# Kernel optimization log

Hardware: AMD Instinct MI355X
Metric: run time of the kernel (lower is better)

Reference implementation:

```python
import jax, jax.numpy as jnp
import numpy as np

D_MODEL = 1024
NUM_HEADS = 16
D_K = D_MODEL // NUM_HEADS
THETA = 10000.0
MAX_SEQ_LEN = 2048
BATCH = 2
SEQ = 2048


def setup_inputs() -> dict:
    key = jax.random.key(0)
    ks = jax.random.split(key, 5)
    std = np.sqrt(2.0 / (D_MODEL + D_MODEL)).astype(np.float32)
    x = jax.random.normal(ks[0], (BATCH, SEQ, D_MODEL), dtype=jnp.float32)
    Wq = jax.random.normal(ks[1], (D_MODEL, D_MODEL), dtype=jnp.float32) * std
    Wk = jax.random.normal(ks[2], (D_MODEL, D_MODEL), dtype=jnp.float32) * std
    Wv = jax.random.normal(ks[3], (D_MODEL, D_MODEL), dtype=jnp.float32) * std
    Wo = jax.random.normal(ks[4], (D_MODEL, D_MODEL), dtype=jnp.float32) * std
    token_positions = jnp.arange(SEQ, dtype=jnp.int32)
    return {"x": x, "token_positions": token_positions,
            "Wq": Wq, "Wk": Wk, "Wv": Wv, "Wo": Wo}


def _rope_tables(positions):
    # freqs: [d_k/2]; angles: [seq, d_k/2]
    freqs = 1.0 / (THETA ** (jnp.arange(0, D_K, 2, dtype=jnp.float32) / D_K))
    angles = positions.astype(jnp.float32)[:, None] * freqs[None, :]
    return jnp.cos(angles), jnp.sin(angles)


def _apply_rope(t, cos, sin):
    # t: [b, h, s, d_k]; cos/sin: [s, d_k/2]; interleaved pair rotation
    x1 = t[..., 0::2]
    x2 = t[..., 1::2]
    r1 = x1 * cos - x2 * sin
    r2 = x1 * sin + x2 * cos
    return jnp.stack([r1, r2], axis=-1).reshape(t.shape)


def reference(x, token_positions, Wq, Wk, Wv, Wo):
    b, s, _ = x.shape
    # projections: y = x W^T
    q = jnp.einsum('bsi,oi->bso', x, Wq)
    k = jnp.einsum('bsi,oi->bso', x, Wk)
    v = jnp.einsum('bsi,oi->bso', x, Wv)
    # split heads: [b, h, s, d]
    q = q.reshape(b, s, NUM_HEADS, D_K).transpose(0, 2, 1, 3)
    k = k.reshape(b, s, NUM_HEADS, D_K).transpose(0, 2, 1, 3)
    v = v.reshape(b, s, NUM_HEADS, D_K).transpose(0, 2, 1, 3)
    cos, sin = _rope_tables(token_positions)
    q = _apply_rope(q, cos, sin)
    k = _apply_rope(k, cos, sin)
    scale = jnp.asarray(D_K, jnp.float32) ** 0.5
    scores = jnp.einsum('bhqd,bhkd->bhqk', q, k) / scale
    causal = jnp.tril(jnp.ones((s, s), dtype=bool))
    scores = jnp.where(causal, scores, -jnp.inf)
    attn = jax.nn.softmax(scores.astype(jnp.float32), axis=-1).astype(scores.dtype)
    out = jnp.einsum('bhqk,bhkd->bhqd', attn, v)
    out = out.transpose(0, 2, 1, 3).reshape(b, s, D_MODEL)
    return jnp.einsum('bsi,oi->bso', out, Wo)
```

## Files before the change

kernel.cpp:

```cpp
#include <hip/hip_runtime.h>
#include <stdint.h>

#define D_MODEL 1024
#define NH      16
#define DKH     64
#define SEQLEN  2048
#define BATCH   2
#define KDIM    1024

typedef __attribute__((ext_vector_type(8))) short          short8;
typedef __attribute__((ext_vector_type(4))) short          bf16x4;
typedef __attribute__((ext_vector_type(8))) unsigned short ushort8;
typedef __attribute__((ext_vector_type(4))) unsigned short usht4;
typedef __attribute__((ext_vector_type(4))) float          f32x4;

#define QSCALE 0.18033688011112042f

__device__ __forceinline__ unsigned short f2bf(float f) {
    union { float f; unsigned u; } v; v.f = f;
    unsigned u = v.u;
    unsigned r = (u + 0x7FFFu + ((u >> 16) & 1u)) >> 16;
    return (unsigned short)r;
}
__device__ __forceinline__ unsigned fbits(float f) {
    union { float f; unsigned u; } v; v.f = f; return v.u;
}

__device__ __forceinline__ void gload_lds16(const unsigned short* g, unsigned short* l) {
    __builtin_amdgcn_global_load_lds(
        (__attribute__((address_space(1))) void*)(g),
        (__attribute__((address_space(3))) void*)(l), 16, 0, 0);
}

__global__ void cvt_all(const float* __restrict__ X,  const float* __restrict__ Wq,
                        const float* __restrict__ Wk, const float* __restrict__ Wv,
                        const float* __restrict__ Wo, const int* __restrict__ pos,
                        unsigned short* __restrict__ Xb,  unsigned short* __restrict__ Wqb,
                        unsigned short* __restrict__ Wkb, unsigned short* __restrict__ Wvb,
                        unsigned short* __restrict__ Wob, float2* __restrict__ tbl) {
    const int z = blockIdx.y;
    if (z == 5) {
        int i = blockIdx.x * 256 + threadIdx.x;
        if (i < 65536) {
            int s = i >> 5, j = i & 31;
            float freq = expf(-((float)(2 * j) * (1.0f / 64.0f)) * 9.210340371976184f);
            float ang = (float)pos[s] * freq;
            float sn, cn;
            sincosf(ang, &sn, &cn);
            tbl[i] = make_float2(cn, sn);
        }
        return;
    }
    const float* src; unsigned short* dst; int n;
    if (z == 0)      { src = X;  dst = Xb;  n = 4194304; }
    else if (z == 1) { src = Wq; dst = Wqb; n = 1048576; }
    else if (z == 2) { src = Wk; dst = Wkb; n = 1048576; }
    else if (z == 3) { src = Wv; dst = Wvb; n = 1048576; }
    else             { src = Wo; dst = Wob; n = 1048576; }
    int i = (blockIdx.x * 256 + threadIdx.x) * 8;
    if (i >= n) return;
    float4 a = *(const float4*)(src + i);
    float4 b = *(const float4*)(src + i + 4);
    ushort8 o;
    o[0] = f2bf(a.x); o[1] = f2bf(a.y); o[2] = f2bf(a.z); o[3] = f2bf(a.w);
    o[4] = f2bf(b.x); o[5] = f2bf(b.y); o[6] = f2bf(b.z); o[7] = f2bf(b.w);
    *(ushort8*)(dst + i) = o;
}

__device__ __forceinline__ void gemm_core_128(
    const unsigned short* __restrict__ A, const unsigned short* __restrict__ W,
    unsigned short* a_lds, unsigned short* b_lds,
    int m0, int n0, f32x4 acc[4][4])
{
    const int tid  = threadIdx.x;
    const int lane = tid & 63;
    const int w    = tid >> 6;
    const int quad = lane >> 4;
    const int l16  = lane & 15;
    const int wm   = w & 1, wn = w >> 1;

    const int row_in = lane >> 3;
    const int cg     = ((lane & 7) ^ row_in) * 8;

    #pragma unroll
    for (int mi = 0; mi < 4; mi++)
        #pragma unroll
        for (int ni = 0; ni < 4; ni++) {
            f32x4 z = {0.f, 0.f, 0.f, 0.f};
            acc[mi][ni] = z;
        }

    const int x7 = l16 & 7;

    for (int kk = 0; kk < KDIM; kk += 64) {
        __syncthreads();
        #pragma unroll
        for (int j = 0; j < 4; ++j) {
            int c = w * 4 + j;
            gload_lds16(A + (size_t)(m0 + c * 8 + row_in) * KDIM + kk + cg, &a_lds[c * 512]);
            gload_lds16(W + (size_t)(n0 + c * 8 + row_in) * KDIM + kk + cg, &b_lds[c * 512]);
        }
        __syncthreads();

        short8 af[2][4], bf[2][4];
        #pragma unroll
        for (int kk2 = 0; kk2 < 2; kk2++)
            #pragma unroll
            for (int i = 0; i < 4; i++) {
                int g = (kk2 * 4 + quad) ^ x7;
                af[kk2][i] = *(const short8*)&a_lds[(wm * 64 + i * 16 + l16) * 64 + g * 8];
                bf[kk2][i] = *(const short8*)&b_lds[(wn * 64 + i * 16 + l16) * 64 + g * 8];
            }
        #pragma unroll
        for (int kk2 = 0; kk2 < 2; kk2++)
            #pragma unroll
            for (int mi = 0; mi < 4; mi++)
                #pragma unroll
                for (int ni = 0; ni < 4; ni++)
                    acc[mi][ni] = __builtin_amdgcn_mfma_f32_16x16x32_bf16(af[kk2][mi], bf[kk2][ni], acc[mi][ni], 0, 0, 0);
    }
}

__global__ __launch_bounds__(256, 2)
void gemm_qkv(const unsigned short* __restrict__ X,
              const unsigned short* __restrict__ Wq,
              const unsigned short* __restrict__ Wk,
              const unsigned short* __restrict__ Wv,
              const float2* __restrict__ tbl,
              unsigned short* __restrict__ q_ws,
              unsigned short* __restrict__ k_ws,
              unsigned short* __restrict__ v_ws)
{
    __shared__ __align__(16) unsigned short a_lds[128 * 64];
    __shared__ __align__(16) unsigned short b_lds[128 * 64];
    __shared__ __align__(16) unsigned short t_lds[32 * 136];

    const int z = blockIdx.z;
    const unsigned short* W = (z == 0) ? Wq : ((z == 1) ? Wk : Wv);
    const int m0 = blockIdx.x * 128, n0 = blockIdx.y * 128;

    f32x4 acc[4][4];
    gemm_core_128(X, W, a_lds, b_lds, m0, n0, acc);

    const int tid  = threadIdx.x;
    const int lane = tid & 63;
    const int w    = tid >> 6;
    const int quad = lane >> 4;
    const int l16  = lane & 15;
    const int wm   = w & 1, wn = w >> 1;

    if (z == 2) {
        const int bx = m0 >> 11;
        const int c_local_w = wn * 16 + l16;
        const int rd_c = tid >> 3;
        const int rd_s = (tid & 7) * 16;
        #pragma unroll
        for (int ni = 0; ni < 4; ni++) {
            __syncthreads();
            #pragma unroll
            for (int mi = 0; mi < 4; mi++) {
                usht4 v4;
                #pragma unroll
                for (int r = 0; r < 4; r++) v4[r] = f2bf(acc[mi][ni][r]);
                *(usht4*)&t_lds[c_local_w * 136 + wm * 64 + mi * 16 + quad * 4] = v4;
            }
            __syncthreads();
            int col = n0 + (rd_c >> 4) * 64 + ni * 16 + (rd_c & 15);
            int h = col >> 6, d = col & 63;
            size_t base = (size_t)(bx * NH + h) * DKH * SEQLEN + (size_t)d * SEQLEN
                        + (m0 & 2047) + rd_s;
            ushort8 x0 = *(ushort8*)&t_lds[rd_c * 136 + rd_s];
            ushort8 x1 = *(ushort8*)&t_lds[rd_c * 136 + rd_s + 8];
            *(ushort8*)&v_ws[base]     = x0;
            *(ushort8*)&v_ws[base + 8] = x1;
        }
    } else {
        unsigned short* dst = (z == 0) ? q_ws : k_ws;
        const float sc = (z == 0) ? QSCALE : 1.0f;
        #pragma unroll
        for (int mi = 0; mi < 4; mi++)
            #pragma unroll
            for (int ni = 0; ni < 4; ni++)
                #pragma unroll
                for (int r = 0; r < 4; r++) {
                    int row = m0 + wm * 64 + mi * 16 + quad * 4 + r;
                    int col = n0 + wn * 64 + ni * 16 + l16;
                    int b = row >> 11, s = row & 2047;
                    int h = col >> 6,  d = col & 63;
                    float val = acc[mi][ni][r];
                    float other = __shfl_xor(val, 1);
                    float2 cs = tbl[s * 32 + (d >> 1)];
                    float rv = (d & 1) ? (other * cs.y + val * cs.x)
                                       : (val * cs.x - other * cs.y);
                    dst[(size_t)(b * NH + h) * SEQLEN * DKH + (size_t)s * DKH + d] =
                        f2bf(rv * sc);
                }
    }
}

__global__ __launch_bounds__(256, 2)
void attn_kernel(const unsigned short* __restrict__ q_ws,
                 const unsigned short* __restrict__ k_ws,
                 const unsigned short* __restrict__ v_ws,
                 unsigned short* __restrict__ ao)
{
    __shared__ __align__(16) unsigned short k_lds[128 * 72];
    __shared__ __align__(16) unsigned short v_lds[64 * 136];

    const int bh  = blockIdx.x;
    const int p   = blockIdx.y;
    const int tid = threadIdx.x, lane = tid & 63, w = tid >> 6;
    const int quad = lane >> 4, l16 = lane & 15;

    const size_t kqbase = (size_t)bh * SEQLEN * DKH;
    const size_t vbase  = (size_t)bh * DKH * SEQLEN;
    const int b = bh >> 4, h = bh & 15;

    const int krow = tid >> 3, kcol = (tid & 7) * 8;
    const int vrow = tid >> 4, vcol = (tid & 15) * 8;

    #pragma unroll
    for (int phase = 0; phase < 2; ++phase) {
        const int qt2 = (phase == 0) ? (15 - p) : p;
        const int q0  = qt2 * 128;
        const int nt  = qt2 + 1;
        const int qwbase = q0 + w * 32;

        short8 aq[2][2];
        #pragma unroll
        for (int st = 0; st < 2; st++)
            #pragma unroll
            for (int kc = 0; kc < 2; kc++)
                aq[st][kc] = *(const short8*)(q_ws + kqbase +
                    (size_t)(qwbase + st * 16 + l16) * DKH + kc * 32 + quad * 8);

        f32x4 o_acc[2][4];
        #pragma unroll
        for (int st = 0; st < 2; st++)
            #pragma unroll
            for (int df = 0; df < 4; df++) { f32x4 z = {0.f,0.f,0.f,0.f}; o_acc[st][df] = z; }
        float lsum[2] = {0.f, 0.f};

        ushort8 kreg[4], vreg[4];
        #pragma unroll
        for (int rr = 0; rr < 4; ++rr) {
            kreg[rr] = *(const ushort8*)(k_ws + kqbase + (size_t)(krow + rr * 32) * DKH + kcol);
            vreg[rr] = *(const ushort8*)(v_ws + vbase + (size_t)(vrow + rr * 16) * SEQLEN + vcol);
        }

        for (int t = 0; t < nt; ++t) {
            const int s0 = t * 128;
            __syncthreads();
            #pragma unroll
            for (int rr = 0; rr < 4; ++rr) {
                *(ushort8*)&k_lds[(krow + rr * 32) * 72 + kcol]  = kreg[rr];
                *(ushort8*)&v_lds[(vrow + rr * 16) * 136 + vcol] = vreg[rr];
            }
            __syncthreads();
            if (t < nt - 1) {
                int s1 = s0 + 128;
                #pragma unroll
                for (int rr = 0; rr < 4; ++rr) {
                    kreg[rr] = *(const ushort8*)(k_ws + kqbase + (size_t)(s1 + krow + rr * 32) * DKH + kcol);
                    vreg[rr] = *(const ushort8*)(v_ws + vbase + (size_t)(vrow + rr * 16) * SEQLEN + s1 + vcol);
                }
            }

            const bool diag = (t == nt - 1);
            #pragma unroll
            for (int nf = 0; nf < 8; nf++) {
                short8 kf0 = *(const short8*)&k_lds[(nf * 16 + l16) * 72 + 0 * 32 + quad * 8];
                short8 kf1 = *(const short8*)&k_lds[(nf * 16 + l16) * 72 + 1 * 32 + quad * 8];
                bf16x4 vf[4];
                #pragma unroll
                for (int df = 0; df < 4; df++)
                    vf[df] = *(const bf16x4*)&v_lds[(df * 16 + l16) * 136 + nf * 16 + quad * 4];

                #pragma unroll
                for (int st = 0; st < 2; st++) {
                    f32x4 s = {0.f,0.f,0.f,0.f};
                    s = __builtin_amdgcn_mfma_f32_16x16x32_bf16(kf0, aq[st][0], s, 0, 0, 0);
                    s = __builtin_amdgcn_mfma_f32_16x16x32_bf16(kf1, aq[st][1], s, 0, 0, 0);

                    if (diag) {
                        int qg = qwbase + st * 16 + l16;
                        int kg = s0 + nf * 16 + quad * 4;
                        #pragma unroll
                        for (int r = 0; r < 4; r++)
                            s[r] = (kg + r <= qg) ? __builtin_amdgcn_exp2f(s[r]) : 0.f;
                    } else {
                        #pragma unroll
                        for (int r = 0; r < 4; r++)
                            s[r] = __builtin_amdgcn_exp2f(s[r]);
                    }
                    lsum[st] += s[0] + s[1] + s[2] + s[3];

                    union { unsigned u[2]; bf16x4 v; } pk;
                    pk.u[0] = __builtin_amdgcn_perm(fbits(s[1]), fbits(s[0]), 0x07060302u);
                    pk.u[1] = __builtin_amdgcn_perm(fbits(s[3]), fbits(s[2]), 0x07060302u);

                    #pragma unroll
                    for (int df = 0; df < 4; df++)
                        o_acc[st][df] = __builtin_amdgcn_mfma_f32_16x16x16bf16_1k(vf[df], pk.v, o_acc[st][df], 0, 0, 0);
                }
            }
        }

        #pragma unroll
        for (int st = 0; st < 2; st++) {
            float rs = lsum[st];
            rs += __shfl_xor(rs, 16);
            rs += __shfl_xor(rs, 32);
            float inv = 1.0f / rs;
            int qg = qwbase + st * 16 + l16;
            #pragma unroll
            for (int df = 0; df < 4; df++) {
                usht4 ov;
                #pragma unroll
                for (int r = 0; r < 4; r++) ov[r] = f2bf(o_acc[st][df][r] * inv);
                *(usht4*)&ao[(size_t)(b * SEQLEN + qg) * D_MODEL + h * DKH + df * 16 + quad * 4] = ov;
            }
        }
    }
}

__global__ __launch_bounds__(256, 2)
void gemm_out(const unsigned short* __restrict__ AO,
              const unsigned short* __restrict__ Wo,
              float* __restrict__ out)
{
    __shared__ __align__(16) unsigned short a_lds[128 * 64];
    __shared__ __align__(16) unsigned short b_lds[128 * 64];

    const int m0 = blockIdx.x * 128, n0 = blockIdx.y * 128;
    f32x4 acc[4][4];
    gemm_core_128(AO, Wo, a_lds, b_lds, m0, n0, acc);

    const int lane = threadIdx.x & 63;
    const int w    = threadIdx.x >> 6;
    const int quad = lane >> 4;
    const int l16  = lane & 15;
    const int wm   = w & 1, wn = w >> 1;

    #pragma unroll
    for (int mi = 0; mi < 4; mi++)
        #pragma unroll
        for (int ni = 0; ni < 4; ni++)
            #pragma unroll
            for (int r = 0; r < 4; r++) {
                int row = m0 + wm * 64 + mi * 16 + quad * 4 + r;
                int col = n0 + wn * 64 + ni * 16 + l16;
                out[(size_t)row * D_MODEL + col] = acc[mi][ni][r];
            }
}

extern "C" void kernel_launch(void* const* d_in, const int* in_sizes, int n_in,
                              void* d_out, int out_size, void* d_ws, size_t ws_size,
                              hipStream_t stream) {
    const float* X  = (const float*)d_in[0];
    const int*   pos = (const int*)d_in[1];
    const float* Wq = (const float*)d_in[2];
    const float* Wk = (const float*)d_in[3];
    const float* Wv = (const float*)d_in[4];
    const float* Wo = (const float*)d_in[5];
    float* out = (float*)d_out;

    unsigned short* Xb  = (unsigned short*)d_ws;
    unsigned short* Wqb = Xb + 4194304;
    unsigned short* Wkb = Wqb + 1048576;
    unsigned short* Wvb = Wkb + 1048576;
    unsigned short* Wob = Wvb + 1048576;
    unsigned short* q_ws = Wob + 1048576;
    unsigned short* k_ws = q_ws + 4194304;
    unsigned short* v_ws = k_ws + 4194304;
    unsigned short* ao   = v_ws + 4194304;
    float2* tbl = (float2*)(ao + 4194304);

    cvt_all<<<dim3(2048, 6), dim3(256), 0, stream>>>(X, Wq, Wk, Wv, Wo, pos,
                                                     Xb, Wqb, Wkb, Wvb, Wob, tbl);
    gemm_qkv<<<dim3(32, 8, 3), dim3(256), 0, stream>>>(Xb, Wqb, Wkb, Wvb, tbl, q_ws, k_ws, v_ws);
    attn_kernel<<<dim3(32, 8), dim3(256), 0, stream>>>(q_ws, k_ws, v_ws, ao);
    gemm_out<<<dim3(32, 8), dim3(256), 0, stream>>>(ao, Wob, out);
}
```

Before: 174.1 us.

## Split attention key tiles across two wave groups with LDS reduction

The attention block grows from 256 to 512 threads. Two groups of four waves each handle half of the 16-key sub-tiles of every 128-key tile for the same query rows, and they share the cooperative K/V tile loads. At the end, the second group writes its partial output accumulators and row sums to shared memory, and the first group adds them and normalizes. The grid has only 256 blocks, so this is meant to double the resident waves per CU and hide more latency. The cost is an extra LDS reduction, two more barriers per query tile, and twice as many threads joining each per-tile barrier.

```diff
diff --git a/kernel.cpp b/kernel.cpp
--- a/kernel.cpp
+++ b/kernel.cpp
@@ -198,19 +198,25 @@
     }
 }
 
-__global__ __launch_bounds__(256, 2)
+__global__ __launch_bounds__(512, 2)
 void attn_kernel(const unsigned short* __restrict__ q_ws,
                  const unsigned short* __restrict__ k_ws,
                  const unsigned short* __restrict__ v_ws,
                  unsigned short* __restrict__ ao)
 {
-    __shared__ __align__(16) unsigned short k_lds[128 * 72];
-    __shared__ __align__(16) unsigned short v_lds[64 * 136];
+    __shared__ __align__(16) unsigned short smem[17920];
+    unsigned short* k_lds = smem;
+    unsigned short* v_lds = smem + 128 * 72;
+    float* redO = (float*)smem;
+    float* redL = redO + 8192;
 
     const int bh  = blockIdx.x;
     const int p   = blockIdx.y;
     const int tid = threadIdx.x, lane = tid & 63, w = tid >> 6;
     const int quad = lane >> 4, l16 = lane & 15;
+    const int g   = w >> 2;
+    const int w4  = w & 3;
+    const int nf0 = g * 4;
 
     const size_t kqbase = (size_t)bh * SEQLEN * DKH;
     const size_t vbase  = (size_t)bh * DKH * SEQLEN;
@@ -224,7 +230,7 @@
         const int qt2 = (phase == 0) ? (15 - p) : p;
         const int q0  = qt2 * 128;
         const int nt  = qt2 + 1;
-        const int qwbase = q0 + w * 32;
+        const int qwbase = q0 + w4 * 32;
 
         short8 aq[2][2];
         #pragma unroll
@@ -241,34 +247,35 @@
             for (int df = 0; df < 4; df++) { f32x4 z = {0.f,0.f,0.f,0.f}; o_acc[st][df] = z; }
         float lsum[2] = {0.f, 0.f};
 
-        ushort8 kreg[4], vreg[4];
-        #pragma unroll
-        for (int rr = 0; rr < 4; ++rr) {
-            kreg[rr] = *(const ushort8*)(k_ws + kqbase + (size_t)(krow + rr * 32) * DKH + kcol);
-            vreg[rr] = *(const ushort8*)(v_ws + vbase + (size_t)(vrow + rr * 16) * SEQLEN + vcol);
+        ushort8 kreg[2], vreg[2];
+        #pragma unroll
+        for (int rr = 0; rr < 2; ++rr) {
+            kreg[rr] = *(const ushort8*)(k_ws + kqbase + (size_t)(krow + rr * 64) * DKH + kcol);
+            vreg[rr] = *(const ushort8*)(v_ws + vbase + (size_t)(vrow + rr * 32) * SEQLEN + vcol);
         }
 
         for (int t = 0; t < nt; ++t) {
             const int s0 = t * 128;
             __syncthreads();
             #pragma unroll
-            for (int rr = 0; rr < 4; ++rr) {
-                *(ushort8*)&k_lds[(krow + rr * 32) * 72 + kcol]  = kreg[rr];
-                *(ushort8*)&v_lds[(vrow + rr * 16) * 136 + vcol] = vreg[rr];
+            for (int rr = 0; rr < 2; ++rr) {
+                *(ushort8*)&k_lds[(krow + rr * 64) * 72 + kcol]  = kreg[rr];
+                *(ushort8*)&v_lds[(vrow + rr * 32) * 136 + vcol] = vreg[rr];
             }
             __syncthreads();
             if (t < nt - 1) {
                 int s1 = s0 + 128;
                 #pragma unroll
-                for (int rr = 0; rr < 4; ++rr) {
-                    kreg[rr] = *(const ushort8*)(k_ws + kqbase + (size_t)(s1 + krow + rr * 32) * DKH + kcol);
-                    vreg[rr] = *(const ushort8*)(v_ws + vbase + (size_t)(vrow + rr * 16) * SEQLEN + s1 + vcol);
+                for (int rr = 0; rr < 2; ++rr) {
+                    kreg[rr] = *(const ushort8*)(k_ws + kqbase + (size_t)(s1 + krow + rr * 64) * DKH + kcol);
+                    vreg[rr] = *(const ushort8*)(v_ws + vbase + (size_t)(vrow + rr * 32) * SEQLEN + s1 + vcol);
                 }
             }
 
             const bool diag = (t == nt - 1);
             #pragma unroll
-            for (int nf = 0; nf < 8; nf++) {
+            for (int nfi = 0; nfi < 4; nfi++) {
+                const int nf = nf0 + nfi;
                 short8 kf0 = *(const short8*)&k_lds[(nf * 16 + l16) * 72 + 0 * 32 + quad * 8];
                 short8 kf1 = *(const short8*)&k_lds[(nf * 16 + l16) * 72 + 1 * 32 + quad * 8];
                 bf16x4 vf[4];
@@ -306,19 +313,37 @@
             }
         }
 
-        #pragma unroll
-        for (int st = 0; st < 2; st++) {
-            float rs = lsum[st];
-            rs += __shfl_xor(rs, 16);
-            rs += __shfl_xor(rs, 32);
-            float inv = 1.0f / rs;
-            int qg = qwbase + st * 16 + l16;
-            #pragma unroll
-            for (int df = 0; df < 4; df++) {
-                usht4 ov;
-                #pragma unroll
-                for (int r = 0; r < 4; r++) ov[r] = f2bf(o_acc[st][df][r] * inv);
-                *(usht4*)&ao[(size_t)(b * SEQLEN + qg) * D_MODEL + h * DKH + df * 16 + quad * 4] = ov;
+        __syncthreads();
+        if (g == 1) {
+            #pragma unroll
+            for (int st = 0; st < 2; st++) {
+                #pragma unroll
+                for (int df = 0; df < 4; df++)
+                    *(f32x4*)&redO[(((w4 * 2 + st) * 4 + df) << 8) + lane * 4] = o_acc[st][df];
+                redL[(w4 * 2 + st) * 64 + lane] = lsum[st];
+            }
+        }
+        __syncthreads();
+        if (g == 0) {
+            #pragma unroll
+            for (int st = 0; st < 2; st++) {
+                #pragma unroll
+                for (int df = 0; df < 4; df++) {
+                    f32x4 o1 = *(const f32x4*)&redO[(((w4 * 2 + st) * 4 + df) << 8) + lane * 4];
+                    o_acc[st][df] += o1;
+                }
+                float rs = lsum[st] + redL[(w4 * 2 + st) * 64 + lane];
+                rs += __shfl_xor(rs, 16);
+                rs += __shfl_xor(rs, 32);
+                float inv = 1.0f / rs;
+                int qg = qwbase + st * 16 + l16;
+                #pragma unroll
+                for (int df = 0; df < 4; df++) {
+                    usht4 ov;
+                    #pragma unroll
+                    for (int r = 0; r < 4; r++) ov[r] = f2bf(o_acc[st][df][r] * inv);
+                    *(usht4*)&ao[(size_t)(b * SEQLEN + qg) * D_MODEL + h * DKH + df * 16 + quad * 4] = ov;
+                }
             }
         }
     }
@@ -379,6 +404,6 @@
     cvt_all<<<dim3(2048, 6), dim3(256), 0, stream>>>(X, Wq, Wk, Wv, Wo, pos,
                                                      Xb, Wqb, Wkb, Wvb, Wob, tbl);
     gemm_qkv<<<dim3(32, 8, 3), dim3(256), 0, stream>>>(Xb, Wqb, Wkb, Wvb, tbl, q_ws, k_ws, v_ws);
-    attn_kernel<<<dim3(32, 8), dim3(256), 0, stream>>>(q_ws, k_ws, v_ws, ao);
+    attn_kernel<<<dim3(32, 8), dim3(512), 0, stream>>>(q_ws, k_ws, v_ws, ao);
     gemm_out<<<dim3(32, 8), dim3(256), 0, stream>>>(ao, Wob, out);
 }
```

Result: faster. 164.9 us (-5.3%).
